# Optimization experiments

Hardware: AMD Instinct MI355X
Metric: run time of the kernel (lower is better)

Reference implementation:

```python
import jax, jax.numpy as jnp
import numpy as np

TOP_K = 4
MAX_NUM_BINS = 32
HIDDEN = 64
STAT_DIM = 4 * (TOP_K + 1)  # 20


def setup_inputs() -> dict:
    key = jax.random.key(0)
    k1, k2, k3, k4 = jax.random.split(key, 4)
    B, L, C = 16, 32768, 80
    scores = jax.random.normal(k1, (B, L, C), dtype=jnp.float32)
    pred_corners = jax.random.normal(k2, (B, L, 4 * (MAX_NUM_BINS + 1)), dtype=jnp.float32)
    # reg_conf MLP params: Dense(20->64) relu, Dense(64->1)
    W1 = jax.random.normal(k3, (STAT_DIM, HIDDEN), dtype=jnp.float32) * (1.0 / np.sqrt(STAT_DIM))
    b1 = jnp.zeros((HIDDEN,), dtype=jnp.float32)
    W2 = jax.random.normal(k4, (HIDDEN, 1), dtype=jnp.float32) * (1.0 / np.sqrt(HIDDEN))
    b2 = jnp.zeros((1,), dtype=jnp.float32)
    return {"scores": scores, "pred_corners": pred_corners,
            "W1": W1, "b1": b1, "W2": W2, "b2": b2}


def reference(scores, pred_corners, W1, b1, W2, b2):
    B, L, _ = pred_corners.shape
    # (B, L, 4, bins+1)
    corners = pred_corners.reshape(B, L, 4, MAX_NUM_BINS + 1)
    prob = jax.nn.softmax(corners, axis=-1)
    # sorted (descending) top-k over bin dim -> (B, L, 4, TOP_K)
    prob_topk, _ = jax.lax.top_k(prob, TOP_K)
    # concat mean -> (B, L, 4, TOP_K+1), then flatten -> (B, L, 20)
    stat = jnp.concatenate(
        [prob_topk, jnp.mean(prob_topk, axis=-1, keepdims=True)], axis=-1)
    stat = stat.reshape(B, L, STAT_DIM)
    # tiny 2-layer MLP -> quality score (B, L, 1)
    h = jax.nn.relu(jnp.einsum("bld,dh->blh", stat, W1) + b1)
    quality = jnp.einsum("blh,ho->blo", h, W2) + b2
    return scores + quality
```

## Files before the change

### kernel.cpp

```cpp
#include <hip/hip_runtime.h>
#include <math.h>

#define TOPK   4
#define NBINS  33
#define CPA    132
#define STATD  20
#define HID    64
#define NCLS   80
#define APB    64
#define BS     256
#define HSTR   68

__global__ __launch_bounds__(BS, 4) void lqe_fused(
    const float* __restrict__ scores,
    const float* __restrict__ corners,
    const float* __restrict__ W1,
    const float* __restrict__ b1,
    const float* __restrict__ W2,
    const float* __restrict__ b2,
    float* __restrict__ out)
{
    __shared__ float s_buf[APB * CPA];
    __shared__ float s_stat[APB * STATD];
    __shared__ float s_q[APB];

    const int tid  = threadIdx.x;
    const int lane = tid & 63;
    const long long aBase = (long long)blockIdx.x * APB;

    {
        const float4* src = (const float4*)(corners + aBase * CPA);
        float4* dst = (float4*)s_buf;
        for (int i = tid; i < (APB * CPA) / 4; i += BS) dst[i] = src[i];
    }
    __syncthreads();

    {
        const int a    = tid >> 2;
        const int side = tid & 3;
        const float* pc = s_buf + a * CPA + side * NBINS;

        float p[NBINS];
        #pragma unroll
        for (int k = 0; k < NBINS; ++k) p[k] = pc[k];

        float m = p[0];
        #pragma unroll
        for (int k = 1; k < NBINS; ++k) m = fmaxf(m, p[k]);

        float s = 0.0f;
        #pragma unroll
        for (int k = 0; k < NBINS; ++k) { p[k] = __expf(p[k] - m); s += p[k]; }

        float t0 = -1.0f, t1 = -1.0f, t2 = -1.0f, t3 = -1.0f;
        #pragma unroll
        for (int k = 0; k < NBINS; ++k) {
            const float v  = p[k];
            const float b0 = fmaxf(t0, v),  c0 = fminf(t0, v);
            const float b1_ = fmaxf(t1, c0), c1 = fminf(t1, c0);
            const float b2_ = fmaxf(t2, c1), c2 = fminf(t2, c1);
            const float b3 = fmaxf(t3, c2);
            t0 = b0; t1 = b1_; t2 = b2_; t3 = b3;
        }

        const float inv = 1.0f / s;
        t0 *= inv; t1 *= inv; t2 *= inv; t3 *= inv;
        const float mean = (t0 + t1 + t2 + t3) * 0.25f;

        float* st = s_stat + a * STATD + side * (TOPK + 1);
        st[0] = t0; st[1] = t1; st[2] = t2; st[3] = t3; st[4] = mean;
    }
    __syncthreads();

    float4 r0, r1, r2, r3, r4;
    {
        const float4* sc = (const float4*)(scores + aBase * NCLS);
        r0 = sc[tid        ];
        r1 = sc[tid + 1*BS ];
        r2 = sc[tid + 2*BS ];
        r3 = sc[tid + 3*BS ];
        r4 = sc[tid + 4*BS ];
    }

    float w1c[STATD];
    #pragma unroll
    for (int d = 0; d < STATD; ++d) w1c[d] = W1[d * HID + lane];
    const float bias = b1[lane];
    const float w2v  = W2[lane];
    const float b2v  = b2[0];

    float* s_h = s_buf;
    {
        const int wave = tid >> 6;
        #pragma unroll
        for (int i = 0; i < APB / 4; ++i) {
            const int a = wave * (APB / 4) + i;
            const float4* sp = (const float4*)(s_stat + a * STATD);
            const float4 s0 = sp[0], s1 = sp[1], s2 = sp[2], s3 = sp[3], s4 = sp[4];
            float acc = bias;
            acc = fmaf(s0.x, w1c[0],  acc); acc = fmaf(s0.y, w1c[1],  acc);
            acc = fmaf(s0.z, w1c[2],  acc); acc = fmaf(s0.w, w1c[3],  acc);
            acc = fmaf(s1.x, w1c[4],  acc); acc = fmaf(s1.y, w1c[5],  acc);
            acc = fmaf(s1.z, w1c[6],  acc); acc = fmaf(s1.w, w1c[7],  acc);
            acc = fmaf(s2.x, w1c[8],  acc); acc = fmaf(s2.y, w1c[9],  acc);
            acc = fmaf(s2.z, w1c[10], acc); acc = fmaf(s2.w, w1c[11], acc);
            acc = fmaf(s3.x, w1c[12], acc); acc = fmaf(s3.y, w1c[13], acc);
            acc = fmaf(s3.z, w1c[14], acc); acc = fmaf(s3.w, w1c[15], acc);
            acc = fmaf(s4.x, w1c[16], acc); acc = fmaf(s4.y, w1c[17], acc);
            acc = fmaf(s4.z, w1c[18], acc); acc = fmaf(s4.w, w1c[19], acc);
            s_h[a * HSTR + lane] = fmaxf(acc, 0.0f) * w2v;
        }
    }
    __syncthreads();

    {
        const int a  = tid >> 2;
        const int qd = tid & 3;
        const float4* hp = (const float4*)(s_h + a * HSTR + qd * 16);
        const float4 h0 = hp[0], h1 = hp[1], h2 = hp[2], h3 = hp[3];
        float v = ((h0.x + h0.y) + (h0.z + h0.w))
                + ((h1.x + h1.y) + (h1.z + h1.w))
                + ((h2.x + h2.y) + (h2.z + h2.w))
                + ((h3.x + h3.y) + (h3.z + h3.w));
        v += __shfl_xor(v, 1, 64);
        v += __shfl_xor(v, 2, 64);
        if (qd == 0) s_q[a] = v + b2v;
    }
    __syncthreads();

    {
        float4* op = (float4*)(out + aBase * NCLS);
        const float q0 = s_q[(tid         ) / (NCLS / 4)];
        const float q1 = s_q[(tid + 1*BS  ) / (NCLS / 4)];
        const float q2 = s_q[(tid + 2*BS  ) / (NCLS / 4)];
        const float q3 = s_q[(tid + 3*BS  ) / (NCLS / 4)];
        const float q4 = s_q[(tid + 4*BS  ) / (NCLS / 4)];
        r0.x += q0; r0.y += q0; r0.z += q0; r0.w += q0;
        r1.x += q1; r1.y += q1; r1.z += q1; r1.w += q1;
        r2.x += q2; r2.y += q2; r2.z += q2; r2.w += q2;
        r3.x += q3; r3.y += q3; r3.z += q3; r3.w += q3;
        r4.x += q4; r4.y += q4; r4.z += q4; r4.w += q4;
        op[tid        ] = r0;
        op[tid + 1*BS ] = r1;
        op[tid + 2*BS ] = r2;
        op[tid + 3*BS ] = r3;
        op[tid + 4*BS ] = r4;
    }
}

extern "C" void kernel_launch(void* const* d_in, const int* in_sizes, int n_in,
                              void* d_out, int out_size, void* d_ws, size_t ws_size,
                              hipStream_t stream) {
    const float* scores  = (const float*)d_in[0];
    const float* corners = (const float*)d_in[1];
    const float* W1      = (const float*)d_in[2];
    const float* b1      = (const float*)d_in[3];
    const float* W2      = (const float*)d_in[4];
    const float* b2      = (const float*)d_in[5];
    float* out = (float*)d_out;
    (void)d_ws; (void)ws_size;

    const int nAnchors = in_sizes[0] / NCLS;
    const int blocks   = nAnchors / APB;

    lqe_fused<<<blocks, BS, 0, stream>>>(scores, corners, W1, b1, W2, b2, out);
}
```

Measured before the change: 506.6 us.

## Process corners in half-block chunks and split per-side softmax across thread pairs

The corners tile is now staged in shared memory in two 32-anchor chunks, halving the LDS buffer, and the launch bound is raised from 4 to 7 blocks per multiprocessor so more blocks can be resident. Each side's 33-bin softmax and top-4 search is split between two threads, with the max, sum and partial top-4 lists merged through wave shuffles and a 4-element sorting network. The scores read is moved to the final add loop, shortening register lifetimes at the cost of less overlap with the MLP phase. The extra chunk loop adds two more barriers and serialises load and compute within a block.

```diff
diff --git a/kernel.cpp b/kernel.cpp
--- a/kernel.cpp
+++ b/kernel.cpp
@@ -8,10 +8,14 @@
 #define HID    64
 #define NCLS   80
 #define APB    64
+#define CHA    32
 #define BS     256
-#define HSTR   68
+#define HSTR   66
+#define SBUF_F (CHA * CPA)
 
-__global__ __launch_bounds__(BS, 4) void lqe_fused(
+#define CE(x, y) { const float _hi = fmaxf(x, y); const float _lo = fminf(x, y); x = _hi; y = _lo; }
+
+__global__ __launch_bounds__(BS, 7) void lqe_fused(
     const float* __restrict__ scores,
     const float* __restrict__ corners,
     const float* __restrict__ W1,
@@ -20,7 +24,7 @@
     const float* __restrict__ b2,
     float* __restrict__ out)
 {
-    __shared__ float s_buf[APB * CPA];
+    __shared__ float s_buf[SBUF_F];
     __shared__ float s_stat[APB * STATD];
     __shared__ float s_q[APB];
 
@@ -28,58 +32,77 @@
     const int lane = tid & 63;
     const long long aBase = (long long)blockIdx.x * APB;
 
-    {
-        const float4* src = (const float4*)(corners + aBase * CPA);
-        float4* dst = (float4*)s_buf;
-        for (int i = tid; i < (APB * CPA) / 4; i += BS) dst[i] = src[i];
-    }
-    __syncthreads();
+    #pragma unroll
+    for (int c = 0; c < 2; ++c) {
+        {
+            const float4* src = (const float4*)(corners + (aBase + c * CHA) * CPA);
+            float4* dst = (float4*)s_buf;
+            const float4 c0 = src[tid         ];
+            const float4 c1 = src[tid + 1 * BS];
+            const float4 c2 = src[tid + 2 * BS];
+            const float4 c3 = src[tid + 3 * BS];
+            float4 c4;
+            const bool tl = tid < (SBUF_F / 4 - 4 * BS);
+            if (tl) c4 = src[tid + 4 * BS];
+            dst[tid         ] = c0;
+            dst[tid + 1 * BS] = c1;
+            dst[tid + 2 * BS] = c2;
+            dst[tid + 3 * BS] = c3;
+            if (tl) dst[tid + 4 * BS] = c4;
+        }
+        __syncthreads();
 
-    {
-        const int a    = tid >> 2;
-        const int side = tid & 3;
-        const float* pc = s_buf + a * CPA + side * NBINS;
+        {
+            const int pid  = tid >> 1;
+            const int h    = tid & 1;
+            const int aL   = pid >> 2;
+            const int side = pid & 3;
+            const float* base = s_buf + aL * CPA + side * NBINS + h * 17;
+            const int nb = 17 - h;
 
-        float p[NBINS];
-        #pragma unroll
-        for (int k = 0; k < NBINS; ++k) p[k] = pc[k];
+            float p[17];
+            #pragma unroll
+            for (int k = 0; k < 17; ++k) p[k] = (k < nb) ? base[k] : -1e30f;
 
-        float m = p[0];
-        #pragma unroll
-        for (int k = 1; k < NBINS; ++k) m = fmaxf(m, p[k]);
+            float m = p[0];
+            #pragma unroll
+            for (int k = 1; k < 17; ++k) m = fmaxf(m, p[k]);
+            m = fmaxf(m, __shfl_xor(m, 1, 64));
 
-        float s = 0.0f;
-        #pragma unroll
-        for (int k = 0; k < NBINS; ++k) { p[k] = __expf(p[k] - m); s += p[k]; }
+            float s = 0.0f;
+            #pragma unroll
+            for (int k = 0; k < 17; ++k) { p[k] = __expf(p[k] - m); s += p[k]; }
+            s += __shfl_xor(s, 1, 64);
 
-        float t0 = -1.0f, t1 = -1.0f, t2 = -1.0f, t3 = -1.0f;
-        #pragma unroll
-        for (int k = 0; k < NBINS; ++k) {
-            const float v  = p[k];
-            const float b0 = fmaxf(t0, v),  c0 = fminf(t0, v);
-            const float b1_ = fmaxf(t1, c0), c1 = fminf(t1, c0);
-            const float b2_ = fmaxf(t2, c1), c2 = fminf(t2, c1);
-            const float b3 = fmaxf(t3, c2);
-            t0 = b0; t1 = b1_; t2 = b2_; t3 = b3;
+            float t0 = -1.0f, t1 = -1.0f, t2 = -1.0f, t3 = -1.0f;
+            #pragma unroll
+            for (int k = 0; k < 17; ++k) {
+                const float v  = p[k];
+                const float b0 = fmaxf(t0, v),   d0 = fminf(t0, v);
+                const float b1_ = fmaxf(t1, d0), d1 = fminf(t1, d0);
+                const float b2_ = fmaxf(t2, d1), d2 = fminf(t2, d1);
+                const float b3 = fmaxf(t3, d2);
+                t0 = b0; t1 = b1_; t2 = b2_; t3 = b3;
+            }
+
+            const float u0 = __shfl_xor(t0, 1, 64);
+            const float u1 = __shfl_xor(t1, 1, 64);
+            const float u2 = __shfl_xor(t2, 1, 64);
+            const float u3 = __shfl_xor(t3, 1, 64);
+            float m0 = fmaxf(t0, u3), m1 = fmaxf(t1, u2);
+            float m2 = fmaxf(t2, u1), m3 = fmaxf(t3, u0);
+            CE(m0, m1); CE(m2, m3); CE(m0, m2); CE(m1, m3); CE(m1, m2);
+
+            const float inv = 1.0f / s;
+            m0 *= inv; m1 *= inv; m2 *= inv; m3 *= inv;
+            const float mean = (m0 + m1 + m2 + m3) * 0.25f;
+
+            if (h == 0) {
+                float* st = s_stat + (c * CHA + aL) * STATD + side * (TOPK + 1);
+                st[0] = m0; st[1] = m1; st[2] = m2; st[3] = m3; st[4] = mean;
+            }
         }
-
-        const float inv = 1.0f / s;
-        t0 *= inv; t1 *= inv; t2 *= inv; t3 *= inv;
-        const float mean = (t0 + t1 + t2 + t3) * 0.25f;
-
-        float* st = s_stat + a * STATD + side * (TOPK + 1);
-        st[0] = t0; st[1] = t1; st[2] = t2; st[3] = t3; st[4] = mean;
-    }
-    __syncthreads();
-
-    float4 r0, r1, r2, r3, r4;
-    {
-        const float4* sc = (const float4*)(scores + aBase * NCLS);
-        r0 = sc[tid        ];
-        r1 = sc[tid + 1*BS ];
-        r2 = sc[tid + 2*BS ];
-        r3 = sc[tid + 3*BS ];
-        r4 = sc[tid + 4*BS ];
+        __syncthreads();
     }
 
     float w1c[STATD];
@@ -116,12 +139,11 @@
     {
         const int a  = tid >> 2;
         const int qd = tid & 3;
-        const float4* hp = (const float4*)(s_h + a * HSTR + qd * 16);
-        const float4 h0 = hp[0], h1 = hp[1], h2 = hp[2], h3 = hp[3];
-        float v = ((h0.x + h0.y) + (h0.z + h0.w))
-                + ((h1.x + h1.y) + (h1.z + h1.w))
-                + ((h2.x + h2.y) + (h2.z + h2.w))
-                + ((h3.x + h3.y) + (h3.z + h3.w));
+        const float2* hp = (const float2*)(s_h + a * HSTR + qd * 16);
+        const float2 h0 = hp[0], h1 = hp[1], h2 = hp[2], h3 = hp[3];
+        const float2 h4 = hp[4], h5 = hp[5], h6 = hp[6], h7 = hp[7];
+        float v = (((h0.x + h0.y) + (h1.x + h1.y)) + ((h2.x + h2.y) + (h3.x + h3.y)))
+                + (((h4.x + h4.y) + (h5.x + h5.y)) + ((h6.x + h6.y) + (h7.x + h7.y)));
         v += __shfl_xor(v, 1, 64);
         v += __shfl_xor(v, 2, 64);
         if (qd == 0) s_q[a] = v + b2v;
@@ -129,22 +151,16 @@
     __syncthreads();
 
     {
+        const float4* sc = (const float4*)(scores + aBase * NCLS);
         float4* op = (float4*)(out + aBase * NCLS);
-        const float q0 = s_q[(tid         ) / (NCLS / 4)];
-        const float q1 = s_q[(tid + 1*BS  ) / (NCLS / 4)];
-        const float q2 = s_q[(tid + 2*BS  ) / (NCLS / 4)];
-        const float q3 = s_q[(tid + 3*BS  ) / (NCLS / 4)];
-        const float q4 = s_q[(tid + 4*BS  ) / (NCLS / 4)];
-        r0.x += q0; r0.y += q0; r0.z += q0; r0.w += q0;
-        r1.x += q1; r1.y += q1; r1.z += q1; r1.w += q1;
-        r2.x += q2; r2.y += q2; r2.z += q2; r2.w += q2;
-        r3.x += q3; r3.y += q3; r3.z += q3; r3.w += q3;
-        r4.x += q4; r4.y += q4; r4.z += q4; r4.w += q4;
-        op[tid        ] = r0;
-        op[tid + 1*BS ] = r1;
-        op[tid + 2*BS ] = r2;
-        op[tid + 3*BS ] = r3;
-        op[tid + 4*BS ] = r4;
+        #pragma unroll
+        for (int r = 0; r < 5; ++r) {
+            const int j = tid + r * BS;
+            const float qv = s_q[j / (NCLS / 4)];
+            float4 v = sc[j];
+            v.x += qv; v.y += qv; v.z += qv; v.w += qv;
+            op[j] = v;
+        }
     }
 }
 
```

Result: no change. 516.7 us (+2.0%).
